# Optimization experiments

Hardware: AMD Instinct MI355X
Metric: run time of the kernel (lower is better)

Reference implementation:

```python
import jax, jax.numpy as jnp
import numpy as np

D_MODEL = 1024
N_HEADS = 16
HEAD_DIM = D_MODEL // N_HEADS


def setup_inputs() -> dict:
    key = jax.random.key(0)
    ks = jax.random.split(key, 9)
    B, L = 2, 2048
    s = 1.0 / np.sqrt(D_MODEL)
    return {
        "x": jax.random.normal(ks[0], (B, L, D_MODEL), dtype=jnp.float32),
        "q_w": jax.random.normal(ks[1], (D_MODEL, D_MODEL), dtype=jnp.float32) * s,
        "q_b": jnp.zeros((D_MODEL,), dtype=jnp.float32),
        "k_w": jax.random.normal(ks[2], (D_MODEL, D_MODEL), dtype=jnp.float32) * s,
        "k_b": jnp.zeros((D_MODEL,), dtype=jnp.float32),
        "v_w": jax.random.normal(ks[3], (D_MODEL, D_MODEL), dtype=jnp.float32) * s,
        "v_b": jnp.zeros((D_MODEL,), dtype=jnp.float32),
        "o_w": jax.random.normal(ks[4], (D_MODEL, D_MODEL), dtype=jnp.float32) * s,
        "o_b": jnp.zeros((D_MODEL,), dtype=jnp.float32),
    }


def _rope_tables(L, dtype):
    # inv_freq: [head_dim//2]
    inv_freq = 1.0 / (10000.0 ** (jnp.arange(0, HEAD_DIM, 2, dtype=dtype) / HEAD_DIM))
    t = jnp.arange(L, dtype=dtype)
    freqs = t[:, None] * inv_freq[None, :]          # [L, hd/2]
    emb = jnp.concatenate([freqs, freqs], axis=-1)  # [L, hd]
    return jnp.cos(emb), jnp.sin(emb)


def _rotate_half(x):
    x1, x2 = x[..., : HEAD_DIM // 2], x[..., HEAD_DIM // 2 :]
    return jnp.concatenate([-x2, x1], axis=-1)


def reference(x, q_w, q_b, k_w, k_b, v_w, v_b, o_w, o_b):
    B, L, D = x.shape
    H, hd = N_HEADS, HEAD_DIM
    # Linear (torch: x @ W.T + b), then split heads -> [B, H, L, hd]
    def proj(w, b):
        y = jnp.einsum("bld,ed->ble", x, w) + b
        return y.reshape(B, L, H, hd).transpose(0, 2, 1, 3)

    q, k, v = proj(q_w, q_b), proj(k_w, k_b), proj(v_w, v_b)

    cos, sin = _rope_tables(L, x.dtype)  # [L, hd] each, broadcast over B,H
    q = q * cos + _rotate_half(q) * sin
    k = k * cos + _rotate_half(k) * sin

    scores = jnp.einsum("bhqd,bhkd->bhqk", q, k) / jnp.sqrt(jnp.asarray(hd, x.dtype))
    attn = jax.nn.softmax(scores, axis=-1)
    out = jnp.einsum("bhqk,bhkd->bhqd", attn, v)
    out = out.transpose(0, 2, 1, 3).reshape(B, L, D)
    return jnp.einsum("bld,ed->ble", out, o_w) + o_b
```

## Files before the change

kernel.cpp:

```cpp
#include <hip/hip_runtime.h>
#include <math.h>

#define SEQ   2048
#define NH    16
#define HD    64
#define DM    1024
#define BATCH 2
#define MROWS (BATCH*SEQ)

typedef __attribute__((ext_vector_type(8))) short short8;
typedef __attribute__((ext_vector_type(4))) float f32x4;
typedef __attribute__((ext_vector_type(16))) float f32x16;
typedef unsigned short ushort;
typedef unsigned int uint;

__device__ __forceinline__ ushort f2bf(float x){
  unsigned int u = __float_as_uint(x);
  unsigned int r = (u + 0x7fffu + ((u>>16)&1u)) >> 16;
  return (ushort)r;
}
__device__ __forceinline__ void gload16(const ushort* g, ushort* l){
  __builtin_amdgcn_global_load_lds(
      (const __attribute__((address_space(1))) unsigned int*)(g),
      (__attribute__((address_space(3))) unsigned int*)(l), 16, 0, 0);
}

__global__ void rope_tables_kernel(float* __restrict__ cosT, float* __restrict__ sinT){
  int idx = blockIdx.x*blockDim.x + threadIdx.x;
  if (idx >= SEQ*32) return;
  int i = idx & 31, l = idx >> 5;
  float e = (float)(2*i) / 64.0f;
  float inv = 1.0f / powf(10000.0f, e);
  float ang = (float)l * inv;
  cosT[idx] = cosf(ang);
  sinT[idx] = sinf(ang);
}

__global__ void cast_all_kernel(
    const float* __restrict__ X,
    const float* __restrict__ wq, const float* __restrict__ wk,
    const float* __restrict__ wv, const float* __restrict__ wo,
    ushort* __restrict__ Xh,
    ushort* __restrict__ hq, ushort* __restrict__ hk,
    ushort* __restrict__ hv, ushort* __restrict__ ho)
{
  int idx = blockIdx.x*blockDim.x + threadIdx.x;
  const float* src; ushort* dh; int off;
  const int NX = (MROWS*DM) >> 2;
  if (idx < NX){ src = X; dh = Xh; off = idx; }
  else {
    int t = idx - NX;
    int sel = t >> 18;
    off = t & 262143;
    src = sel==0 ? wq : sel==1 ? wk : sel==2 ? wv : wo;
    dh  = sel==0 ? hq : sel==1 ? hk : sel==2 ? hv : ho;
  }
  float4 v = ((const float4*)src)[off];
  uint2 hp;
  hp.x = (unsigned)f2bf(v.x) | ((unsigned)f2bf(v.y)<<16);
  hp.y = (unsigned)f2bf(v.z) | ((unsigned)f2bf(v.w)<<16);
  ((uint2*)dh)[off] = hp;
}

__global__ __launch_bounds__(256) void gemm_qkv_mfma(
    const ushort* __restrict__ Xh,
    const ushort* __restrict__ Whq, const ushort* __restrict__ Whk, const ushort* __restrict__ Whv,
    const float* __restrict__ bq, const float* __restrict__ bk, const float* __restrict__ bv,
    const float* __restrict__ cosT, const float* __restrict__ sinT,
    ushort* __restrict__ Qb, ushort* __restrict__ Kb, ushort* __restrict__ Vb)
{
  __shared__ __align__(16) ushort As[128*64];
  __shared__ __align__(16) ushort Bs[128*64];
  const int tid = threadIdx.x, w = tid>>6, lane = tid&63;
  const int c = lane & 15, g = lane >> 4;
  const int wr = w >> 1, wc = w & 1;
  const int m0   = blockIdx.x * 128;
  const int ncat = blockIdx.y * 128;
  const int which = ncat >> 10;
  const int n0    = ncat & 1023;
  const ushort* Bhi = which==0 ? Whq : which==1 ? Whk : Whv;
  const float*  bias= which==0 ? bq  : which==1 ? bk  : bv;

  const int srow = lane >> 3;
  const int scol = ((lane & 7) ^ srow) << 3;

  f32x4 acc[4][4] = {};
  for (int k0 = 0; k0 < DM; k0 += 64){
    __syncthreads();
    #pragma unroll
    for (int i=0;i<4;i++){
      const int rb = w*32 + i*8;
      gload16(Xh  + (size_t)(m0 + rb + srow)*DM + k0 + scol, &As[rb*64]);
      gload16(Bhi + (size_t)(n0 + rb + srow)*DM + k0 + scol, &Bs[rb*64]);
    }
    __syncthreads();
    #pragma unroll
    for (int kc=0;kc<2;kc++){
      short8 a[4], b[4];
      #pragma unroll
      for (int m=0;m<4;m++){
        int row = wr*64 + m*16 + c;
        a[m] = *(const short8*)&As[row*64 + ((((kc<<2)+g) ^ (row&7))<<3)];
      }
      #pragma unroll
      for (int n=0;n<4;n++){
        int row = wc*64 + n*16 + c;
        b[n] = *(const short8*)&Bs[row*64 + ((((kc<<2)+g) ^ (row&7))<<3)];
      }
      #pragma unroll
      for (int m=0;m<4;m++)
        #pragma unroll
        for (int n=0;n<4;n++)
          acc[m][n] = __builtin_amdgcn_mfma_f32_16x16x32_bf16(a[m], b[n], acc[m][n], 0,0,0);
    }
  }

  const int hh = (n0 + wc*64) >> 6;
  ushort* Out = which==0 ? Qb : which==1 ? Kb : Vb;
  #pragma unroll
  for (int m=0;m<4;m++){
    #pragma unroll
    for (int r=0;r<4;r++){
      int mrow = m0 + wr*64 + m*16 + 4*g + r;
      int bb = mrow >> 11, l = mrow & (SEQ-1);
      size_t obase = (((size_t)bb*NH + hh)*SEQ + l)*HD;
      size_t vbase = (((size_t)bb*NH + hh)*HD)*SEQ + l;
      #pragma unroll
      for (int n=0;n<2;n++){
        int d1 = n*16 + c, d2 = d1 + 32;
        float v1 = acc[m][n  ][r] + bias[hh*64 + d1];
        float v2 = acc[m][n+2][r] + bias[hh*64 + d2];
        if (which < 2){
          float co = cosT[l*32 + d1], si = sinT[l*32 + d1];
          float o1 = v1*co - v2*si;
          float o2 = v2*co + v1*si;
          if (which == 0){ o1 *= 0.125f; o2 *= 0.125f; }
          Out[obase + d1] = f2bf(o1);
          Out[obase + d2] = f2bf(o2);
        } else {
          Out[vbase + (size_t)d1*SEQ] = f2bf(v1);
          Out[vbase + (size_t)d2*SEQ] = f2bf(v2);
        }
      }
    }
  }
}

__global__ __launch_bounds__(256) void flash_mfma_kernel(
    const ushort* __restrict__ Qb, const ushort* __restrict__ Kb,
    const ushort* __restrict__ VTg, ushort* __restrict__ AOh)
{
  __shared__ __align__(16) ushort Ks[2][64*64];
  __shared__ __align__(16) ushort Vs[2][64*64];

  const int tid  = threadIdx.x;
  const int w    = tid >> 6;
  const int lane = tid & 63;
  const int c    = lane & 31;
  const int h    = lane >> 5;
  const int hd = blockIdx.y, b = blockIdx.z;
  const int bh = b*NH + hd;
  const int q0 = blockIdx.x*128 + w*32;

  const int srow   = lane >> 3;
  const int sgran8 = ((lane & 7) ^ srow) << 3;
  const int rb0 = w*16, rb1 = w*16 + 8;

  const ushort* Kbase = Kb  + (size_t)bh*SEQ*HD;
  const ushort* Vbase = VTg + (size_t)bh*HD*SEQ;

  const ushort* Qrow = Qb + ((size_t)bh*SEQ + q0 + c)*HD + 8*h;
  short8 qf[4];
  #pragma unroll
  for (int kc=0;kc<4;kc++) qf[kc] = *(const short8*)(Qrow + kc*16);

  short8 ones;
  #pragma unroll
  for (int i=0;i<8;i++) ones[i] = (short)0x3F80;

  f32x16 oacc[2] = {};
  f32x16 sacc = {};

  gload16(Kbase + (size_t)(rb0 + srow)*HD + sgran8, &Ks[0][rb0*64]);
  gload16(Kbase + (size_t)(rb1 + srow)*HD + sgran8, &Ks[0][rb1*64]);
  gload16(Vbase + (size_t)(rb0 + srow)*SEQ + sgran8, &Vs[0][rb0*64]);
  gload16(Vbase + (size_t)(rb1 + srow)*SEQ + sgran8, &Vs[0][rb1*64]);
  __syncthreads();

  int buf = 0;
  for (int t0 = 0; t0 < SEQ; t0 += 64){
    if (t0 + 64 < SEQ){
      const int nb = buf ^ 1, t1 = t0 + 64;
      gload16(Kbase + (size_t)(t1 + rb0 + srow)*HD + sgran8, &Ks[nb][rb0*64]);
      gload16(Kbase + (size_t)(t1 + rb1 + srow)*HD + sgran8, &Ks[nb][rb1*64]);
      gload16(Vbase + (size_t)(rb0 + srow)*SEQ + t1 + sgran8, &Vs[nb][rb0*64]);
      gload16(Vbase + (size_t)(rb1 + srow)*SEQ + t1 + sgran8, &Vs[nb][rb1*64]);
    }

    #pragma unroll
    for (int kb=0; kb<2; kb++){
      f32x16 s = {};
      __builtin_amdgcn_s_setprio(1);
      #pragma unroll
      for (int kc=0;kc<4;kc++){
        int row = kb*32 + c;
        short8 kf = *(const short8*)&Ks[buf][row*64 + (((2*kc + h) ^ (row&7))<<3)];
        s = __builtin_amdgcn_mfma_f32_32x32x16_bf16(kf, qf[kc], s, 0,0,0);
      }
      __builtin_amdgcn_s_setprio(0);

      uint pk[8];
      #pragma unroll
      for (int i=0;i<8;i++){
        float p0 = __expf(s[2*i]);
        float p1 = __expf(s[2*i+1]);
        asm("v_cvt_pk_bf16_f32 %0, %1, %2" : "=v"(pk[i]) : "v"(p0), "v"(p1));
      }
      asm volatile("v_permlane32_swap_b32 %0, %1" : "+v"(pk[0]), "+v"(pk[2]));
      asm volatile("v_permlane32_swap_b32 %0, %1" : "+v"(pk[1]), "+v"(pk[3]));
      asm volatile("v_permlane32_swap_b32 %0, %1" : "+v"(pk[4]), "+v"(pk[6]));
      asm volatile("v_permlane32_swap_b32 %0, %1" : "+v"(pk[5]), "+v"(pk[7]));
      short8 pa0, pa1;
      ((uint*)&pa0)[0]=pk[0]; ((uint*)&pa0)[1]=pk[1]; ((uint*)&pa0)[2]=pk[2]; ((uint*)&pa0)[3]=pk[3];
      ((uint*)&pa1)[0]=pk[4]; ((uint*)&pa1)[1]=pk[5]; ((uint*)&pa1)[2]=pk[6]; ((uint*)&pa1)[3]=pk[7];

      __builtin_amdgcn_s_setprio(1);
      #pragma unroll
      for (int db=0; db<2; db++){
        int vrow = db*32 + c;
        short8 v0 = *(const short8*)&Vs[buf][vrow*64 + (((4*kb     + h) ^ (vrow&7))<<3)];
        short8 v1 = *(const short8*)&Vs[buf][vrow*64 + (((4*kb + 2 + h) ^ (vrow&7))<<3)];
        oacc[db] = __builtin_amdgcn_mfma_f32_32x32x16_bf16(pa0, v0, oacc[db], 0,0,0);
        oacc[db] = __builtin_amdgcn_mfma_f32_32x32x16_bf16(pa1, v1, oacc[db], 0,0,0);
      }
      sacc = __builtin_amdgcn_mfma_f32_32x32x16_bf16(pa0, ones, sacc, 0,0,0);
      sacc = __builtin_amdgcn_mfma_f32_32x32x16_bf16(pa1, ones, sacc, 0,0,0);
      __builtin_amdgcn_s_setprio(0);
    }

    __syncthreads();
    buf ^= 1;
  }

  float inv[16];
  #pragma unroll
  for (int r=0;r<16;r++) inv[r] = 1.0f / sacc[r];
  #pragma unroll
  for (int db=0; db<2; db++){
    #pragma unroll
    for (int r=0;r<16;r++){
      int q = q0 + (r&3) + 8*(r>>2) + 4*h;
      AOh[((size_t)b*SEQ + q)*DM + hd*HD + db*32 + c] = f2bf(oacc[db][r] * inv[r]);
    }
  }
}

__global__ __launch_bounds__(256) void gemm_o_mfma(
    const ushort* __restrict__ AOh, const ushort* __restrict__ Who,
    const float* __restrict__ bo, float* __restrict__ Y)
{
  __shared__ __align__(16) ushort As[128*64];
  __shared__ __align__(16) ushort Bs[128*64];
  const int tid = threadIdx.x, w = tid>>6, lane = tid&63;
  const int c = lane & 15, g = lane >> 4;
  const int wr = w >> 1, wc = w & 1;
  const int m0 = blockIdx.x * 128;
  const int n0 = blockIdx.y * 128;

  const int srow = lane >> 3;
  const int scol = ((lane & 7) ^ srow) << 3;

  f32x4 acc[4][4] = {};
  for (int k0 = 0; k0 < DM; k0 += 64){
    __syncthreads();
    #pragma unroll
    for (int i=0;i<4;i++){
      const int rb = w*32 + i*8;
      gload16(AOh + (size_t)(m0 + rb + srow)*DM + k0 + scol, &As[rb*64]);
      gload16(Who + (size_t)(n0 + rb + srow)*DM + k0 + scol, &Bs[rb*64]);
    }
    __syncthreads();
    #pragma unroll
    for (int kc=0;kc<2;kc++){
      short8 a[4], b[4];
      #pragma unroll
      for (int m=0;m<4;m++){
        int row = wr*64 + m*16 + c;
        a[m] = *(const short8*)&As[row*64 + ((((kc<<2)+g) ^ (row&7))<<3)];
      }
      #pragma unroll
      for (int n=0;n<4;n++){
        int row = wc*64 + n*16 + c;
        b[n] = *(const short8*)&Bs[row*64 + ((((kc<<2)+g) ^ (row&7))<<3)];
      }
      #pragma unroll
      for (int m=0;m<4;m++)
        #pragma unroll
        for (int n=0;n<4;n++)
          acc[m][n] = __builtin_amdgcn_mfma_f32_16x16x32_bf16(a[m], b[n], acc[m][n], 0,0,0);
    }
  }

  #pragma unroll
  for (int m=0;m<4;m++){
    #pragma unroll
    for (int r=0;r<4;r++){
      int mrow = m0 + wr*64 + m*16 + 4*g + r;
      #pragma unroll
      for (int n=0;n<4;n++){
        int ncol = n0 + wc*64 + n*16 + c;
        Y[(size_t)mrow*DM + ncol] = acc[m][n][r] + bo[ncol];
      }
    }
  }
}

extern "C" void kernel_launch(void* const* d_in, const int* in_sizes, int n_in,
                              void* d_out, int out_size, void* d_ws, size_t ws_size,
                              hipStream_t stream)
{
  const float* x  = (const float*)d_in[0];
  const float* qw = (const float*)d_in[1];
  const float* qb = (const float*)d_in[2];
  const float* kw = (const float*)d_in[3];
  const float* kb = (const float*)d_in[4];
  const float* vw = (const float*)d_in[5];
  const float* vb = (const float*)d_in[6];
  const float* ow = (const float*)d_in[7];
  const float* ob = (const float*)d_in[8];
  float* out = (float*)d_out;

  const size_t NE = (size_t)MROWS*DM;
  const size_t WE = (size_t)DM*DM;
  float* cosT = (float*)d_ws;
  float* sinT = cosT + SEQ*32;
  ushort* p = (ushort*)(sinT + SEQ*32);
  ushort* Xh  = p;            p += NE;
  ushort* Whq = p;            p += WE;
  ushort* Whk = p;            p += WE;
  ushort* Whv = p;            p += WE;
  ushort* Who = p;            p += WE;
  ushort* Qb  = p;            p += NE;
  ushort* Kb  = p;            p += NE;
  ushort* Vb  = p;            p += NE;
  ushort* AOh = p;            p += NE;

  hipLaunchKernelGGL(rope_tables_kernel, dim3((SEQ*32+255)/256), dim3(256), 0, stream, cosT, sinT);
  hipLaunchKernelGGL(cast_all_kernel, dim3((NE/4 + WE)/256), dim3(256), 0, stream,
                     x, qw, kw, vw, ow, Xh, Whq, Whk, Whv, Who);
  hipLaunchKernelGGL(gemm_qkv_mfma, dim3(MROWS/128, 3072/128), dim3(256), 0, stream,
                     Xh, Whq, Whk, Whv, qb, kb, vb, cosT, sinT, Qb, Kb, Vb);
  hipLaunchKernelGGL(flash_mfma_kernel, dim3(SEQ/128, NH, BATCH), dim3(256), 0, stream,
                     Qb, Kb, Vb, AOh);
  hipLaunchKernelGGL(gemm_o_mfma, dim3(MROWS/128, DM/128), dim3(256), 0, stream,
                     AOh, Who, ob, out);
}
```

Before: 133.5 us.

## Store flash K/V tiles in fragment-order LDS layout and remap blocks for XCD locality

```diff
diff --git a/kernel.cpp b/kernel.cpp
--- a/kernel.cpp
+++ b/kernel.cpp
@@ -150,21 +150,20 @@
     const ushort* __restrict__ Qb, const ushort* __restrict__ Kb,
     const ushort* __restrict__ VTg, ushort* __restrict__ AOh)
 {
-  __shared__ __align__(16) ushort Ks[2][64*64];
-  __shared__ __align__(16) ushort Vs[2][64*64];
+  __shared__ __align__(16) ushort Ks[2][8][512];
+  __shared__ __align__(16) ushort Vs[2][8][512];
 
   const int tid  = threadIdx.x;
   const int w    = tid >> 6;
   const int lane = tid & 63;
   const int c    = lane & 31;
   const int h    = lane >> 5;
-  const int hd = blockIdx.y, b = blockIdx.z;
+
+  const int hw = blockIdx.x;
+  const int lg = (hw & 7)*64 + (hw >> 3);
+  const int bx = lg & 15, hd = (lg >> 4) & 15, b = lg >> 8;
   const int bh = b*NH + hd;
-  const int q0 = blockIdx.x*128 + w*32;
-
-  const int srow   = lane >> 3;
-  const int sgran8 = ((lane & 7) ^ srow) << 3;
-  const int rb0 = w*16, rb1 = w*16 + 8;
+  const int q0 = bx*128 + w*32;
 
   const ushort* Kbase = Kb  + (size_t)bh*SEQ*HD;
   const ushort* Vbase = VTg + (size_t)bh*HD*SEQ;
@@ -181,20 +180,20 @@
   f32x16 oacc[2] = {};
   f32x16 sacc = {};
 
-  gload16(Kbase + (size_t)(rb0 + srow)*HD + sgran8, &Ks[0][rb0*64]);
-  gload16(Kbase + (size_t)(rb1 + srow)*HD + sgran8, &Ks[0][rb1*64]);
-  gload16(Vbase + (size_t)(rb0 + srow)*SEQ + sgran8, &Vs[0][rb0*64]);
-  gload16(Vbase + (size_t)(rb1 + srow)*SEQ + sgran8, &Vs[0][rb1*64]);
+  #define STAGE(bf, t0) { \
+    _Pragma("unroll") for (int i_=0;i_<2;i_++){ \
+      int n_ = 2*w + i_; \
+      gload16(Kbase + (size_t)((t0) + (n_>>2)*32 + c)*HD + (n_&3)*16 + 8*h, &Ks[bf][n_][0]); \
+      gload16(Vbase + (size_t)((n_>>2)*32 + c)*SEQ + (t0) + ((n_>>1)&1)*32 + (n_&1)*16 + 8*h, &Vs[bf][n_][0]); \
+    } }
+
+  STAGE(0, 0)
   __syncthreads();
 
   int buf = 0;
   for (int t0 = 0; t0 < SEQ; t0 += 64){
     if (t0 + 64 < SEQ){
-      const int nb = buf ^ 1, t1 = t0 + 64;
-      gload16(Kbase + (size_t)(t1 + rb0 + srow)*HD + sgran8, &Ks[nb][rb0*64]);
-      gload16(Kbase + (size_t)(t1 + rb1 + srow)*HD + sgran8, &Ks[nb][rb1*64]);
-      gload16(Vbase + (size_t)(rb0 + srow)*SEQ + t1 + sgran8, &Vs[nb][rb0*64]);
-      gload16(Vbase + (size_t)(rb1 + srow)*SEQ + t1 + sgran8, &Vs[nb][rb1*64]);
+      STAGE(buf ^ 1, t0 + 64)
     }
 
     #pragma unroll
@@ -203,8 +202,7 @@
       __builtin_amdgcn_s_setprio(1);
       #pragma unroll
       for (int kc=0;kc<4;kc++){
-        int row = kb*32 + c;
-        short8 kf = *(const short8*)&Ks[buf][row*64 + (((2*kc + h) ^ (row&7))<<3)];
+        short8 kf = *(const short8*)&Ks[buf][kb*4+kc][lane*8];
         s = __builtin_amdgcn_mfma_f32_32x32x16_bf16(kf, qf[kc], s, 0,0,0);
       }
       __builtin_amdgcn_s_setprio(0);
@@ -227,9 +225,8 @@
       __builtin_amdgcn_s_setprio(1);
       #pragma unroll
       for (int db=0; db<2; db++){
-        int vrow = db*32 + c;
-        short8 v0 = *(const short8*)&Vs[buf][vrow*64 + (((4*kb     + h) ^ (vrow&7))<<3)];
-        short8 v1 = *(const short8*)&Vs[buf][vrow*64 + (((4*kb + 2 + h) ^ (vrow&7))<<3)];
+        short8 v0 = *(const short8*)&Vs[buf][db*4 + kb*2 + 0][lane*8];
+        short8 v1 = *(const short8*)&Vs[buf][db*4 + kb*2 + 1][lane*8];
         oacc[db] = __builtin_amdgcn_mfma_f32_32x32x16_bf16(pa0, v0, oacc[db], 0,0,0);
         oacc[db] = __builtin_amdgcn_mfma_f32_32x32x16_bf16(pa1, v1, oacc[db], 0,0,0);
       }
@@ -241,6 +238,7 @@
     __syncthreads();
     buf ^= 1;
   }
+  #undef STAGE
 
   float inv[16];
   #pragma unroll
@@ -350,7 +348,7 @@
                      x, qw, kw, vw, ow, Xh, Whq, Whk, Whv, Who);
   hipLaunchKernelGGL(gemm_qkv_mfma, dim3(MROWS/128, 3072/128), dim3(256), 0, stream,
                      Xh, Whq, Whk, Whv, qb, kb, vb, cosT, sinT, Qb, Kb, Vb);
-  hipLaunchKernelGGL(flash_mfma_kernel, dim3(SEQ/128, NH, BATCH), dim3(256), 0, stream,
+  hipLaunchKernelGGL(flash_mfma_kernel, dim3(512), dim3(256), 0, stream,
                      Qb, Kb, Vb, AOh);
   hipLaunchKernelGGL(gemm_o_mfma, dim3(MROWS/128, DM/128), dim3(256), 0, stream,
                      AOh, Who, ob, out);
```

Measured after the change: 139.1 us. 1.04x slower.
